# Kernel tuning notes

Measured on AMD Instinct MI355X. Metric: run time of the kernel, lower is better.

## Reference

```python
import jax, jax.numpy as jnp
import numpy as np

B, A, NN, G, F, L, MAXZ = 8, 1024, 64, 25, 128, 3, 100
CUTOFF = 5.0

def ssp(x):
    # shifted softplus: ln(0.5*e^x + 0.5) = softplus(x) - ln(2)
    return jax.nn.softplus(x) - jnp.log(2.0)

def setup_inputs() -> dict:
    key = jax.random.key(0)
    ks = jax.random.split(key, 10)
    atomic_numbers = jax.random.randint(ks[0], (B, A), 0, MAXZ)
    positions = jax.random.normal(ks[1], (B, A, 3), dtype=jnp.float32) * 3.0
    cell = jnp.zeros((B, 3, 3), dtype=jnp.float32)
    cell_offset = jnp.zeros((B, A, NN, 3), dtype=jnp.float32)
    neighbors = jax.random.randint(ks[2], (B, A, NN), 0, A)
    neighbor_mask = jnp.ones((B, A, NN), dtype=jnp.float32)
    s = 0.05
    emb = jax.random.normal(ks[3], (MAXZ, F), dtype=jnp.float32) * s
    emb = emb.at[0].set(0.0)  # padding_idx=0
    return dict(
        atomic_numbers=atomic_numbers, positions=positions, cell=cell,
        cell_offset=cell_offset, neighbors=neighbors, neighbor_mask=neighbor_mask,
        emb=emb,
        fw1=jax.random.normal(ks[4], (L, G, F), dtype=jnp.float32) * s,
        fb1=jnp.zeros((L, F), dtype=jnp.float32),
        fw2=jax.random.normal(ks[5], (L, F, F), dtype=jnp.float32) * s,
        fb2=jnp.zeros((L, F), dtype=jnp.float32),
        in2f_w=jax.random.normal(ks[6], (L, F, F), dtype=jnp.float32) * s,
        f2out_w=jax.random.normal(ks[7], (L, F, F), dtype=jnp.float32) * s,
        f2out_b=jnp.zeros((L, F), dtype=jnp.float32),
        dense_w=jax.random.normal(ks[8], (L, F, F), dtype=jnp.float32) * s,
        dense_b=jnp.zeros((L, F), dtype=jnp.float32),
    )

def reference(atomic_numbers, positions, cell, cell_offset, neighbors,
              neighbor_mask, emb, fw1, fb1, fw2, fb2, in2f_w, f2out_w,
              f2out_b, dense_w, dense_b):
    bidx = jnp.arange(B)[:, None, None]
    # embedding lookup [B,A,F]
    x = emb[atomic_numbers]
    # AtomDistances: gather neighbor positions, add cell offsets, norm
    pos_j = positions[bidx, neighbors]                       # [B,A,NN,3]
    dv = pos_j - positions[:, :, None, :] + jnp.einsum('bank,bkc->banc', cell_offset, cell)
    d2 = jnp.sum(dv * dv, axis=-1)                           # [B,A,NN]
    r_ij = jnp.where(d2 > 0, jnp.sqrt(jnp.where(d2 > 0, d2, 1.0)), 0.0)
    # GaussianSmearing on [0, cutoff] with G gaussians
    offsets = jnp.linspace(0.0, CUTOFF, G)
    width = offsets[1] - offsets[0]
    coeff = -0.5 / (width * width)
    f_ij = jnp.exp(coeff * (r_ij[..., None] - offsets) ** 2)  # [B,A,NN,G]
    mask = neighbor_mask[..., None]                           # [B,A,NN,1]
    for l in range(L):
        # filter-generating network on expanded distances -> [B,A,NN,F]
        W = ssp(f_ij @ fw1[l] + fb1[l]) @ fw2[l] + fb2[l]
        # cfconv: in2f (no bias), gather neighbor features, mul, masked sum
        y = x @ in2f_w[l]                                     # [B,A,F]
        yj = y[bidx, neighbors]                               # [B,A,NN,F]
        v = jnp.sum(yj * W * mask, axis=2)                    # [B,A,F]
        v = ssp(v @ f2out_w[l] + f2out_b[l])
        # interaction output dense (linear)
        v = v @ dense_w[l] + dense_b[l]
        x = x + v
    return x
```

## Files before the change

### kernel.cpp

```cpp
#include <hip/hip_runtime.h>
#include <hip/hip_bf16.h>
#include <math.h>

#define B_ 8
#define A_ 1024
#define NN_ 64
#define G_ 25
#define F_ 128
#define L_ 3
#define TG_ 4096
#define TGP_ (TG_ + 8)

typedef __hip_bfloat16 bf16;
typedef __bf16 bf16x8 __attribute__((ext_vector_type(8)));
typedef __bf16 bf16x4 __attribute__((ext_vector_type(4)));
typedef float floatx4 __attribute__((ext_vector_type(4)));
#define MFMA16 __builtin_amdgcn_mfma_f32_16x16x32_bf16

__device__ __forceinline__ float sspfast(float x){
  return __logf(0.5f*__expf(x) + 0.5f);
}
__device__ __forceinline__ float ldsel(const void* p, long long i, int isbf){
  return isbf ? __bfloat162float(((const bf16*)p)[i]) : ((const float*)p)[i];
}
__device__ __forceinline__ int sniff_bf16(const void* pos){
  const unsigned* raw = (const unsigned*)pos;
  unsigned w = raw[threadIdx.x & 63];
  unsigned e = (w >> 7) & 0xFF;
  return __popcll(__ballot(e >= 118 && e <= 132)) >= 32;
}

__global__ __launch_bounds__(256) void k_setup(
    const void* emb, const void* fb1, const void* fb2, const void* f2ob,
    const void* db,  const void* fw1, const void* fw2, const void* f2ow,
    const void* dw,  const void* in2f, const void* pos,
    float* c_emb, float* c_fb1, float* c_fb2, float* c_f2ob, float* c_db,
    __bf16* fw1tb, __bf16* fw2tb, __bf16* f2owtb, __bf16* dwtb, __bf16* in2ftb)
{
  int isbf = sniff_bf16(pos);
  int idx = blockIdx.x*256 + threadIdx.x;
  if(idx < 12800){ c_emb[idx] = ldsel(emb, idx, isbf); return; }
  if(idx < 13184){ c_fb1[idx-12800] = ldsel(fb1, idx-12800, isbf); return; }
  if(idx < 13568){ c_fb2[idx-13184] = ldsel(fb2, idx-13184, isbf); return; }
  if(idx < 13952){ c_f2ob[idx-13568] = ldsel(f2ob, idx-13568, isbf); return; }
  if(idx < 14336){ c_db[idx-13952] = ldsel(db, idx-13952, isbf); return; }
  if(idx < 26624){
    int i = idx - 14336;
    int l = i >> 12; int rem = i & 4095; int f = rem >> 5; int k = rem & 31;
    float v = (k < G_) ? ldsel(fw1, (long long)l*G_*F_ + k*F_ + f, isbf) : 0.0f;
    fw1tb[i] = (__bf16)v;
    return;
  }
  {
    int i = idx - 26624;
    int which = i / 49152; int r = i - which*49152;
    int l = r >> 14; int rem = r & 16383; int f = rem >> 7; int k = rem & 127;
    const void* src = (which==0) ? fw2 : (which==1) ? f2ow : (which==2) ? dw : in2f;
    __bf16* dst = (which==0) ? fw2tb : (which==1) ? f2owtb : (which==2) ? dwtb : in2ftb;
    dst[r] = (__bf16)ldsel(src, (long long)l*F_*F_ + k*F_ + f, isbf);
  }
}

__global__ __launch_bounds__(256, 4) void k_build(
    const __bf16* __restrict__ fw1tb, const float* __restrict__ fb1g,
    const __bf16* __restrict__ fw2tb, const float* __restrict__ fb2g,
    __bf16* __restrict__ wtabb,
    const int* __restrict__ z, const float* __restrict__ c_emb,
    const __bf16* __restrict__ in2ftb, float* __restrict__ xws,
    __bf16* __restrict__ ybf,
    const void* pos, const void* cell, const void* celloff,
    const int* __restrict__ nbr, const void* maskg,
    int2* __restrict__ pair)
{
  __shared__ __align__(16) unsigned char smem[22528];
  int t = threadIdx.x;
  int lane = t & 63, wid = t >> 6, c = lane & 15, quad = lane >> 4;
  int wb = wid*32;

  if(blockIdx.x >= 448){
    int isbf = sniff_bf16(pos);
    int p = (blockIdx.x - 448)*256 + t;
    int m = p >> 6;
    int b = m >> 10;
    int j = nbr[p];
    long long pi = (long long)m*3, pj = (long long)(b*A_+j)*3;
    long long co = (long long)p*3, ce = (long long)b*9;
    float o0 = ldsel(celloff,co+0,isbf), o1 = ldsel(celloff,co+1,isbf), o2 = ldsel(celloff,co+2,isbf);
    float d2 = 0.0f;
    #pragma unroll
    for(int cc=0;cc<3;cc++){
      float off = o0*ldsel(cell,ce+cc,isbf) + o1*ldsel(cell,ce+3+cc,isbf) + o2*ldsel(cell,ce+6+cc,isbf);
      float dv = ldsel(pos,pj+cc,isbf) - ldsel(pos,pi+cc,isbf) + off;
      d2 += dv*dv;
    }
    float r = (d2 > 0.0f) ? sqrtf(d2) : 0.0f;
    float msk = ldsel(maskg, p, isbf);
    int i = (int)(r * ((float)TG_ / 8.0f) + 0.5f);
    if(i > TG_-1) i = TG_-1;
    if(msk < 0.5f) i = TG_;
    int2 pr;
    pr.x = i * F_;
    pr.y = (b*A_ + j) * F_;
    pair[p] = pr;
    return;
  }

  if(blockIdx.x < 192){
    __bf16* s_h1  = (__bf16*)smem;
    __bf16* s_fij = (__bf16*)(smem + 17408);
    int layer = blockIdx.x >> 6;
    int row0  = (blockIdx.x & 63) * 64;
    __bf16* T = wtabb + (long long)layer*TGP_*F_;

    if((blockIdx.x & 63) == 0 && t < F_)
      T[(long long)TG_*F_ + t] = (__bf16)0.0f;

    const float dr = 8.0f / (float)TG_;
    const float width = 5.0f/24.0f;
    const float coeff = -0.5f/(width*width);
    for(int i=t;i<NN_*40;i+=256){
      int n = i/40, g = i - n*40;
      float val = 0.0f;
      if(g < G_){
        float rg = (float)(row0 + n) * dr;
        float d = rg - (float)g*width;
        val = __expf(coeff*d*d);
      }
      s_fij[i] = (__bf16)val;
    }
    __syncthreads();

    {
      const __bf16* fw1l = fw1tb + layer*F_*32;
      bf16x8 a0 = *(const bf16x8*)(fw1l + (wb + c)*32 + quad*8);
      bf16x8 a1 = *(const bf16x8*)(fw1l + (wb + 16 + c)*32 + quad*8);
      floatx4 bias0 = *(const floatx4*)(fb1g + layer*F_ + wb + quad*4);
      floatx4 bias1 = *(const floatx4*)(fb1g + layer*F_ + wb + 16 + quad*4);
      #pragma unroll
      for(int nt=0;nt<4;nt++){
        bf16x8 bfr = *(const bf16x8*)(s_fij + (nt*16 + c)*40 + quad*8);
        floatx4 z4 = {0.f,0.f,0.f,0.f};
        floatx4 acc0 = MFMA16(a0, bfr, z4, 0,0,0);
        floatx4 acc1 = MFMA16(a1, bfr, z4, 0,0,0);
        bf16x4 h0, h1v;
        #pragma unroll
        for(int r=0;r<4;r++){
          h0[r]  = (__bf16)sspfast(acc0[r] + bias0[r]);
          h1v[r] = (__bf16)sspfast(acc1[r] + bias1[r]);
        }
        *(bf16x4*)(s_h1 + (nt*16+c)*136 + wb + quad*4)      = h0;
        *(bf16x4*)(s_h1 + (nt*16+c)*136 + wb + 16 + quad*4) = h1v;
      }
    }
    __syncthreads();

    {
      const __bf16* fw2l = fw2tb + layer*F_*F_;
      bf16x8 aw0[4], aw1[4];
      #pragma unroll
      for(int kt=0;kt<4;kt++){
        aw0[kt] = *(const bf16x8*)(fw2l + (wb + c)*F_ + kt*32 + quad*8);
        aw1[kt] = *(const bf16x8*)(fw2l + (wb + 16 + c)*F_ + kt*32 + quad*8);
      }
      floatx4 ba0 = *(const floatx4*)(fb2g + layer*F_ + wb + quad*4);
      floatx4 ba1 = *(const floatx4*)(fb2g + layer*F_ + wb + 16 + quad*4);
      #pragma unroll
      for(int nt=0; nt<4; nt++){
        bf16x8 bh[4];
        #pragma unroll
        for(int kt=0;kt<4;kt++)
          bh[kt] = *(const bf16x8*)(s_h1 + (nt*16 + c)*136 + kt*32 + quad*8);
        floatx4 acc0 = {0.f,0.f,0.f,0.f};
        floatx4 acc1 = {0.f,0.f,0.f,0.f};
        #pragma unroll
        for(int kt=0;kt<4;kt++){
          acc0 = MFMA16(aw0[kt], bh[kt], acc0, 0,0,0);
          acc1 = MFMA16(aw1[kt], bh[kt], acc1, 0,0,0);
        }
        int row = row0 + nt*16 + c;
        bf16x4 o0, o1;
        #pragma unroll
        for(int r=0;r<4;r++){
          o0[r] = (__bf16)(acc0[r] + ba0[r]);
          o1[r] = (__bf16)(acc1[r] + ba1[r]);
        }
        *(bf16x4*)(T + (long long)row*F_ + wb + quad*4)      = o0;
        *(bf16x4*)(T + (long long)row*F_ + wb + 16 + quad*4) = o1;
      }
    }
    return;
  }

  {
    __bf16* s_a = (__bf16*)smem;
    int row0 = (blockIdx.x - 192)*32;
    #pragma unroll
    for(int i=0;i<2;i++){
      int ch = t + i*256, row = ch >> 4, col8 = ch & 15;
      const float* src = c_emb + (long long)z[row0+row]*F_ + col8*8;
      float4 a4 = ((const float4*)src)[0];
      float4 b4 = ((const float4*)src)[1];
      float* xd = xws + (long long)(row0+row)*F_ + col8*8;
      ((float4*)xd)[0] = a4; ((float4*)xd)[1] = b4;
      bf16x8 v = {(__bf16)a4.x,(__bf16)a4.y,(__bf16)a4.z,(__bf16)a4.w,
                  (__bf16)b4.x,(__bf16)b4.y,(__bf16)b4.z,(__bf16)b4.w};
      *(bf16x8*)(s_a + row*136 + col8*8) = v;
    }
    __syncthreads();
    bf16x8 aw0[4], aw1[4];
    #pragma unroll
    for(int kt=0;kt<4;kt++){
      aw0[kt] = *(const bf16x8*)(in2ftb + (wb + c)*F_ + kt*32 + quad*8);
      aw1[kt] = *(const bf16x8*)(in2ftb + (wb + 16 + c)*F_ + kt*32 + quad*8);
    }
    #pragma unroll
    for(int nt=0; nt<2; nt++){
      bf16x8 bh[4];
      #pragma unroll
      for(int kt=0;kt<4;kt++)
        bh[kt] = *(const bf16x8*)(s_a + (nt*16 + c)*136 + kt*32 + quad*8);
      floatx4 acc0 = {0.f,0.f,0.f,0.f};
      floatx4 acc1 = {0.f,0.f,0.f,0.f};
      #pragma unroll
      for(int kt=0;kt<4;kt++){
        acc0 = MFMA16(aw0[kt], bh[kt], acc0, 0,0,0);
        acc1 = MFMA16(aw1[kt], bh[kt], acc1, 0,0,0);
      }
      int row = row0 + nt*16 + c;
      bf16x4 o0, o1;
      #pragma unroll
      for(int r=0;r<4;r++){ o0[r] = (__bf16)acc0[r]; o1[r] = (__bf16)acc1[r]; }
      *(bf16x4*)(ybf + (long long)row*F_ + wb + quad*4)      = o0;
      *(bf16x4*)(ybf + (long long)row*F_ + wb + 16 + quad*4) = o1;
    }
  }
}

__global__ __launch_bounds__(256, 2) void k_layer(
    const __bf16* __restrict__ yin, const int2* __restrict__ pairg,
    const __bf16* __restrict__ Tb, float* __restrict__ xws,
    const __bf16* __restrict__ f2owl, const float* __restrict__ f2obl,
    const __bf16* __restrict__ dwl,  const float* __restrict__ dbl,
    const __bf16* __restrict__ in2fnext, __bf16* __restrict__ yout,
    void* __restrict__ dout, const void* __restrict__ pos,
    int has_next, int write_out)
{
  __shared__ __align__(16) int2  s_pair[16*NN_];
  __shared__ __align__(16) float s_vpf[4*16*128];
  __shared__ __align__(16) __bf16 s_ga[16*136];
  __shared__ __align__(16) __bf16 s_gb[16*136];

  int t = threadIdx.x;
  int bid = (int)blockIdx.x;
  int m0 = ((bid & 7) * 64 + (bid >> 3)) * 16;
  int lane = t & 63, wid = t >> 6, c = lane & 15, quad = lane >> 4;
  int isbf = sniff_bf16(pos);

  {
    const int2* src = pairg + (long long)m0*NN_;
    for(int i=t;i<16*NN_;i+=256) s_pair[i] = src[i];
  }
  __syncthreads();

  int fsl = t & 15;
  int grp = t >> 4;
  int f8 = fsl*8;
  #pragma unroll 2
  for(int a=0;a<16;a++){
    float v0=0.f,v1=0.f,v2=0.f,v3=0.f,v4=0.f,v5=0.f,v6=0.f,v7=0.f;
    #pragma unroll
    for(int jj=0;jj<4;jj++){
      int2 pr = s_pair[a*NN_ + jj*16 + grp];
      bf16x8 T = *(const bf16x8*)(Tb + pr.x + f8);
      bf16x8 Y = *(const bf16x8*)(yin + pr.y + f8);
      v0 += (float)T[0]*(float)Y[0];
      v1 += (float)T[1]*(float)Y[1];
      v2 += (float)T[2]*(float)Y[2];
      v3 += (float)T[3]*(float)Y[3];
      v4 += (float)T[4]*(float)Y[4];
      v5 += (float)T[5]*(float)Y[5];
      v6 += (float)T[6]*(float)Y[6];
      v7 += (float)T[7]*(float)Y[7];
    }
    v0 += __shfl_xor(v0,16); v1 += __shfl_xor(v1,16);
    v2 += __shfl_xor(v2,16); v3 += __shfl_xor(v3,16);
    v4 += __shfl_xor(v4,16); v5 += __shfl_xor(v5,16);
    v6 += __shfl_xor(v6,16); v7 += __shfl_xor(v7,16);
    v0 += __shfl_xor(v0,32); v1 += __shfl_xor(v1,32);
    v2 += __shfl_xor(v2,32); v3 += __shfl_xor(v3,32);
    v4 += __shfl_xor(v4,32); v5 += __shfl_xor(v5,32);
    v6 += __shfl_xor(v6,32); v7 += __shfl_xor(v7,32);
    if(lane < 16){
      float* dst = s_vpf + (wid*16 + a)*128 + lane*8;
      floatx4 lo = {v0,v1,v2,v3}, hi = {v4,v5,v6,v7};
      *(floatx4*)dst = lo;
      *(floatx4*)(dst+4) = hi;
    }
  }
  __syncthreads();
  {
    int a0 = t >> 5, q = t & 31;
    #pragma unroll
    for(int h=0; h<2; h++){
      int a = a0 + h*8;
      floatx4 p0 = *(const floatx4*)(s_vpf + (0*16+a)*128 + q*4);
      floatx4 p1 = *(const floatx4*)(s_vpf + (1*16+a)*128 + q*4);
      floatx4 p2 = *(const floatx4*)(s_vpf + (2*16+a)*128 + q*4);
      floatx4 p3 = *(const floatx4*)(s_vpf + (3*16+a)*128 + q*4);
      bf16x4 o;
      #pragma unroll
      for(int r=0;r<4;r++)
        o[r] = (__bf16)(p0[r]+p1[r]+p2[r]+p3[r]);
      *(bf16x4*)(s_ga + a*136 + q*4) = o;
    }
  }
  __syncthreads();

  int wb = wid*32;
  {
    bf16x8 aw0[4], aw1[4];
    #pragma unroll
    for(int kt=0;kt<4;kt++){
      aw0[kt] = *(const bf16x8*)(f2owl + (wb + c)*F_ + kt*32 + quad*8);
      aw1[kt] = *(const bf16x8*)(f2owl + (wb + 16 + c)*F_ + kt*32 + quad*8);
    }
    floatx4 ba0 = *(const floatx4*)(f2obl + wb + quad*4);
    floatx4 ba1 = *(const floatx4*)(f2obl + wb + 16 + quad*4);
    bf16x8 bh[4];
    #pragma unroll
    for(int kt=0;kt<4;kt++)
      bh[kt] = *(const bf16x8*)(s_ga + c*136 + kt*32 + quad*8);
    floatx4 acc0 = {0.f,0.f,0.f,0.f};
    floatx4 acc1 = {0.f,0.f,0.f,0.f};
    #pragma unroll
    for(int kt=0;kt<4;kt++){
      acc0 = MFMA16(aw0[kt], bh[kt], acc0, 0,0,0);
      acc1 = MFMA16(aw1[kt], bh[kt], acc1, 0,0,0);
    }
    bf16x4 o0, o1;
    #pragma unroll
    for(int r=0;r<4;r++){
      o0[r] = (__bf16)sspfast(acc0[r] + ba0[r]);
      o1[r] = (__bf16)sspfast(acc1[r] + ba1[r]);
    }
    *(bf16x4*)(s_gb + c*136 + wb + quad*4)      = o0;
    *(bf16x4*)(s_gb + c*136 + wb + 16 + quad*4) = o1;
  }
  __syncthreads();

  {
    bf16x8 aw0[4], aw1[4];
    #pragma unroll
    for(int kt=0;kt<4;kt++){
      aw0[kt] = *(const bf16x8*)(dwl + (wb + c)*F_ + kt*32 + quad*8);
      aw1[kt] = *(const bf16x8*)(dwl + (wb + 16 + c)*F_ + kt*32 + quad*8);
    }
    floatx4 ba0 = *(const floatx4*)(dbl + wb + quad*4);
    floatx4 ba1 = *(const floatx4*)(dbl + wb + 16 + quad*4);
    bf16x8 bh[4];
    #pragma unroll
    for(int kt=0;kt<4;kt++)
      bh[kt] = *(const bf16x8*)(s_gb + c*136 + kt*32 + quad*8);
    floatx4 acc0 = {0.f,0.f,0.f,0.f};
    floatx4 acc1 = {0.f,0.f,0.f,0.f};
    #pragma unroll
    for(int kt=0;kt<4;kt++){
      acc0 = MFMA16(aw0[kt], bh[kt], acc0, 0,0,0);
      acc1 = MFMA16(aw1[kt], bh[kt], acc1, 0,0,0);
    }
    int rowL = m0 + c;
    float* xp0 = xws + (long long)rowL*F_ + wb + quad*4;
    float* xp1 = xws + (long long)rowL*F_ + wb + 16 + quad*4;
    float4 x0 = *(const float4*)xp0;
    float4 x1 = *(const float4*)xp1;
    float4 xn0 = {x0.x+acc0[0]+ba0[0], x0.y+acc0[1]+ba0[1],
                  x0.z+acc0[2]+ba0[2], x0.w+acc0[3]+ba0[3]};
    float4 xn1 = {x1.x+acc1[0]+ba1[0], x1.y+acc1[1]+ba1[1],
                  x1.z+acc1[2]+ba1[2], x1.w+acc1[3]+ba1[3]};
    bf16x4 s0 = {(__bf16)xn0.x,(__bf16)xn0.y,(__bf16)xn0.z,(__bf16)xn0.w};
    bf16x4 s1 = {(__bf16)xn1.x,(__bf16)xn1.y,(__bf16)xn1.z,(__bf16)xn1.w};
    *(bf16x4*)(s_ga + c*136 + wb + quad*4)      = s0;
    *(bf16x4*)(s_ga + c*136 + wb + 16 + quad*4) = s1;
    *(float4*)xp0 = xn0;
    *(float4*)xp1 = xn1;
    if(write_out){
      long long gi0 = (long long)rowL*F_ + wb + quad*4;
      long long gi1 = (long long)rowL*F_ + wb + 16 + quad*4;
      if(isbf){
        *(bf16x4*)((bf16*)dout + gi0) = s0;
        *(bf16x4*)((bf16*)dout + gi1) = s1;
      }else{
        *(float4*)((float*)dout + gi0) = xn0;
        *(float4*)((float*)dout + gi1) = xn1;
      }
    }
  }
  if(!has_next) return;
  __syncthreads();

  {
    bf16x8 aw0[4], aw1[4];
    #pragma unroll
    for(int kt=0;kt<4;kt++){
      aw0[kt] = *(const bf16x8*)(in2fnext + (wb + c)*F_ + kt*32 + quad*8);
      aw1[kt] = *(const bf16x8*)(in2fnext + (wb + 16 + c)*F_ + kt*32 + quad*8);
    }
    bf16x8 bh[4];
    #pragma unroll
    for(int kt=0;kt<4;kt++)
      bh[kt] = *(const bf16x8*)(s_ga + c*136 + kt*32 + quad*8);
    floatx4 acc0 = {0.f,0.f,0.f,0.f};
    floatx4 acc1 = {0.f,0.f,0.f,0.f};
    #pragma unroll
    for(int kt=0;kt<4;kt++){
      acc0 = MFMA16(aw0[kt], bh[kt], acc0, 0,0,0);
      acc1 = MFMA16(aw1[kt], bh[kt], acc1, 0,0,0);
    }
    int row = m0 + c;
    bf16x4 o0, o1;
    #pragma unroll
    for(int r=0;r<4;r++){ o0[r] = (__bf16)acc0[r]; o1[r] = (__bf16)acc1[r]; }
    *(bf16x4*)(yout + (long long)row*F_ + wb + quad*4)      = o0;
    *(bf16x4*)(yout + (long long)row*F_ + wb + 16 + quad*4) = o1;
  }
}

extern "C" void kernel_launch(void* const* d_in, const int* in_sizes, int n_in,
                              void* d_out, int out_size, void* d_ws, size_t ws_size,
                              hipStream_t stream){
  const int*  z       = (const int*)d_in[0];
  const void* pos     = d_in[1];
  const void* cell    = d_in[2];
  const void* celloff = d_in[3];
  const int*  nbr     = (const int*)d_in[4];
  const void* mask    = d_in[5];
  const void* emb     = d_in[6];
  const void* fw1     = d_in[7];
  const void* fb1     = d_in[8];
  const void* fw2     = d_in[9];
  const void* fb2     = d_in[10];
  const void* in2f    = d_in[11];
  const void* f2ow    = d_in[12];
  const void* f2ob    = d_in[13];
  const void* dw      = d_in[14];
  const void* db      = d_in[15];

  float* base = (float*)d_ws;
  float* c_emb  = base + 16;
  float* c_fb1  = c_emb + 12800;
  float* c_fb2  = c_fb1 + 384;
  float* c_f2ob = c_fb2 + 384;
  float* c_db   = c_f2ob + 384;
  __bf16* fw1tb  = (__bf16*)(c_db + 384);
  __bf16* fw2tb  = (__bf16*)(base + 20496);
  __bf16* f2owtb = (__bf16*)(base + 45072);
  __bf16* dwtb   = (__bf16*)(base + 69648);
  __bf16* in2ftb = (__bf16*)(base + 94224);
  float*  xws   = base + 118800;
  __bf16* ybf0  = (__bf16*)(base + 1167376);
  __bf16* ybf1  = (__bf16*)(base + 1691664);
  int2*   pair  = (int2*)(base + 2215952);
  __bf16* wtabb = (__bf16*)(base + 3264528);

  k_setup<<<872, 256, 0, stream>>>(emb, fb1, fb2, f2ob, db,
                                   fw1, fw2, f2ow, dw, in2f, pos,
                                   c_emb, c_fb1, c_fb2, c_f2ob, c_db,
                                   fw1tb, fw2tb, f2owtb, dwtb, in2ftb);
  k_build<<<2496, 256, 0, stream>>>(fw1tb, c_fb1, fw2tb, c_fb2, wtabb,
                                    z, c_emb, in2ftb, xws, ybf0,
                                    pos, cell, celloff, nbr, mask, pair);

  __bf16* ycur = ybf0;
  __bf16* ynext = ybf1;
  for(int l=0;l<L_;l++){
    k_layer<<<(B_*A_)/16, 256, 0, stream>>>(ycur, pair,
                                            wtabb + (long long)l*TGP_*F_, xws,
                                            f2owtb + l*F_*F_, c_f2ob + l*F_,
                                            dwtb + l*F_*F_,  c_db + l*F_,
                                            in2ftb + (l < L_-1 ? (l+1)*F_*F_ : 0), ynext,
                                            d_out, pos,
                                            (l < L_-1) ? 1 : 0, (l == L_-1) ? 1 : 0);
    __bf16* tmp = ycur; ycur = ynext; ynext = tmp;
  }
}
```

Before: 174.2 us.

## Store filter table and neighbor features as scaled FP8 to halve gather bytes

The precomputed distance-filter table and the per-atom in2f features move from bf16 to FP8 (scaled by fixed factors 32 and 64), and the layer kernel unpacks them with packed fp8-to-f32 conversions before the multiply-accumulate. The sum is rescaled by the inverse factor before the f2out GEMM. This halves the bytes of the random neighbor gather, which dominates each layer kernel, at the cost of much lower precision and a risk of exceeding the accuracy tolerance. The extra conversion instructions add ALU work.

```diff
diff --git a/kernel.cpp b/kernel.cpp
--- a/kernel.cpp
+++ b/kernel.cpp
@@ -10,11 +10,15 @@
 #define L_ 3
 #define TG_ 4096
 #define TGP_ (TG_ + 8)
+#define SCT 32.0f
+#define SCY 64.0f
+#define INVS (1.0f/(32.0f*64.0f))
 
 typedef __hip_bfloat16 bf16;
 typedef __bf16 bf16x8 __attribute__((ext_vector_type(8)));
 typedef __bf16 bf16x4 __attribute__((ext_vector_type(4)));
 typedef float floatx4 __attribute__((ext_vector_type(4)));
+typedef float floatx2 __attribute__((ext_vector_type(2)));
 #define MFMA16 __builtin_amdgcn_mfma_f32_16x16x32_bf16
 
 __device__ __forceinline__ float sspfast(float x){
@@ -28,6 +32,11 @@
   unsigned w = raw[threadIdx.x & 63];
   unsigned e = (w >> 7) & 0xFF;
   return __popcll(__ballot(e >= 118 && e <= 132)) >= 32;
+}
+__device__ __forceinline__ unsigned int pack4_fp8(float a, float b, float c, float d){
+  int r = __builtin_amdgcn_cvt_pk_fp8_f32(a, b, 0, false);
+  r = __builtin_amdgcn_cvt_pk_fp8_f32(c, d, r, true);
+  return (unsigned int)r;
 }
 
 __global__ __launch_bounds__(256) void k_setup(
@@ -64,10 +73,10 @@
 __global__ __launch_bounds__(256, 4) void k_build(
     const __bf16* __restrict__ fw1tb, const float* __restrict__ fb1g,
     const __bf16* __restrict__ fw2tb, const float* __restrict__ fb2g,
-    __bf16* __restrict__ wtabb,
+    unsigned char* __restrict__ wtab8,
     const int* __restrict__ z, const float* __restrict__ c_emb,
     const __bf16* __restrict__ in2ftb, float* __restrict__ xws,
-    __bf16* __restrict__ ybf,
+    unsigned char* __restrict__ y8,
     const void* pos, const void* cell, const void* celloff,
     const int* __restrict__ nbr, const void* maskg,
     int2* __restrict__ pair)
@@ -110,10 +119,10 @@
     __bf16* s_fij = (__bf16*)(smem + 17408);
     int layer = blockIdx.x >> 6;
     int row0  = (blockIdx.x & 63) * 64;
-    __bf16* T = wtabb + (long long)layer*TGP_*F_;
-
-    if((blockIdx.x & 63) == 0 && t < F_)
-      T[(long long)TG_*F_ + t] = (__bf16)0.0f;
+    unsigned char* T8 = wtab8 + (long long)layer*TGP_*F_;
+
+    if((blockIdx.x & 63) == 0 && t < 32)
+      *(unsigned int*)(T8 + (long long)TG_*F_ + t*4) = 0u;
 
     const float dr = 8.0f / (float)TG_;
     const float width = 5.0f/24.0f;
@@ -178,14 +187,12 @@
           acc1 = MFMA16(aw1[kt], bh[kt], acc1, 0,0,0);
         }
         int row = row0 + nt*16 + c;
-        bf16x4 o0, o1;
-        #pragma unroll
-        for(int r=0;r<4;r++){
-          o0[r] = (__bf16)(acc0[r] + ba0[r]);
-          o1[r] = (__bf16)(acc1[r] + ba1[r]);
-        }
-        *(bf16x4*)(T + (long long)row*F_ + wb + quad*4)      = o0;
-        *(bf16x4*)(T + (long long)row*F_ + wb + 16 + quad*4) = o1;
+        unsigned int w0 = pack4_fp8((acc0[0]+ba0[0])*SCT, (acc0[1]+ba0[1])*SCT,
+                                    (acc0[2]+ba0[2])*SCT, (acc0[3]+ba0[3])*SCT);
+        unsigned int w1 = pack4_fp8((acc1[0]+ba1[0])*SCT, (acc1[1]+ba1[1])*SCT,
+                                    (acc1[2]+ba1[2])*SCT, (acc1[3]+ba1[3])*SCT);
+        *(unsigned int*)(T8 + (long long)row*F_ + wb + quad*4)      = w0;
+        *(unsigned int*)(T8 + (long long)row*F_ + wb + 16 + quad*4) = w1;
       }
     }
     return;
@@ -227,21 +234,20 @@
         acc1 = MFMA16(aw1[kt], bh[kt], acc1, 0,0,0);
       }
       int row = row0 + nt*16 + c;
-      bf16x4 o0, o1;
-      #pragma unroll
-      for(int r=0;r<4;r++){ o0[r] = (__bf16)acc0[r]; o1[r] = (__bf16)acc1[r]; }
-      *(bf16x4*)(ybf + (long long)row*F_ + wb + quad*4)      = o0;
-      *(bf16x4*)(ybf + (long long)row*F_ + wb + 16 + quad*4) = o1;
+      unsigned int w0 = pack4_fp8(acc0[0]*SCY, acc0[1]*SCY, acc0[2]*SCY, acc0[3]*SCY);
+      unsigned int w1 = pack4_fp8(acc1[0]*SCY, acc1[1]*SCY, acc1[2]*SCY, acc1[3]*SCY);
+      *(unsigned int*)(y8 + (long long)row*F_ + wb + quad*4)      = w0;
+      *(unsigned int*)(y8 + (long long)row*F_ + wb + 16 + quad*4) = w1;
     }
   }
 }
 
 __global__ __launch_bounds__(256, 2) void k_layer(
-    const __bf16* __restrict__ yin, const int2* __restrict__ pairg,
-    const __bf16* __restrict__ Tb, float* __restrict__ xws,
+    const unsigned char* __restrict__ yin, const int2* __restrict__ pairg,
+    const unsigned char* __restrict__ Tb, float* __restrict__ xws,
     const __bf16* __restrict__ f2owl, const float* __restrict__ f2obl,
     const __bf16* __restrict__ dwl,  const float* __restrict__ dbl,
-    const __bf16* __restrict__ in2fnext, __bf16* __restrict__ yout,
+    const __bf16* __restrict__ in2fnext, unsigned char* __restrict__ yout,
     void* __restrict__ dout, const void* __restrict__ pos,
     int has_next, int write_out)
 {
@@ -271,16 +277,24 @@
     #pragma unroll
     for(int jj=0;jj<4;jj++){
       int2 pr = s_pair[a*NN_ + jj*16 + grp];
-      bf16x8 T = *(const bf16x8*)(Tb + pr.x + f8);
-      bf16x8 Y = *(const bf16x8*)(yin + pr.y + f8);
-      v0 += (float)T[0]*(float)Y[0];
-      v1 += (float)T[1]*(float)Y[1];
-      v2 += (float)T[2]*(float)Y[2];
-      v3 += (float)T[3]*(float)Y[3];
-      v4 += (float)T[4]*(float)Y[4];
-      v5 += (float)T[5]*(float)Y[5];
-      v6 += (float)T[6]*(float)Y[6];
-      v7 += (float)T[7]*(float)Y[7];
+      uint2 Tw = *(const uint2*)(Tb + pr.x + f8);
+      uint2 Yw = *(const uint2*)(yin + pr.y + f8);
+      floatx2 t0 = __builtin_amdgcn_cvt_pk_f32_fp8((int)Tw.x, false);
+      floatx2 t1 = __builtin_amdgcn_cvt_pk_f32_fp8((int)Tw.x, true);
+      floatx2 t2 = __builtin_amdgcn_cvt_pk_f32_fp8((int)Tw.y, false);
+      floatx2 t3 = __builtin_amdgcn_cvt_pk_f32_fp8((int)Tw.y, true);
+      floatx2 u0 = __builtin_amdgcn_cvt_pk_f32_fp8((int)Yw.x, false);
+      floatx2 u1 = __builtin_amdgcn_cvt_pk_f32_fp8((int)Yw.x, true);
+      floatx2 u2 = __builtin_amdgcn_cvt_pk_f32_fp8((int)Yw.y, false);
+      floatx2 u3 = __builtin_amdgcn_cvt_pk_f32_fp8((int)Yw.y, true);
+      v0 += t0[0]*u0[0];
+      v1 += t0[1]*u0[1];
+      v2 += t1[0]*u1[0];
+      v3 += t1[1]*u1[1];
+      v4 += t2[0]*u2[0];
+      v5 += t2[1]*u2[1];
+      v6 += t3[0]*u3[0];
+      v7 += t3[1]*u3[1];
     }
     v0 += __shfl_xor(v0,16); v1 += __shfl_xor(v1,16);
     v2 += __shfl_xor(v2,16); v3 += __shfl_xor(v3,16);
@@ -310,7 +324,7 @@
       bf16x4 o;
       #pragma unroll
       for(int r=0;r<4;r++)
-        o[r] = (__bf16)(p0[r]+p1[r]+p2[r]+p3[r]);
+        o[r] = (__bf16)((p0[r]+p1[r]+p2[r]+p3[r]) * INVS);
       *(bf16x4*)(s_ga + a*136 + q*4) = o;
     }
   }
@@ -417,11 +431,10 @@
       acc1 = MFMA16(aw1[kt], bh[kt], acc1, 0,0,0);
     }
     int row = m0 + c;
-    bf16x4 o0, o1;
-    #pragma unroll
-    for(int r=0;r<4;r++){ o0[r] = (__bf16)acc0[r]; o1[r] = (__bf16)acc1[r]; }
-    *(bf16x4*)(yout + (long long)row*F_ + wb + quad*4)      = o0;
-    *(bf16x4*)(yout + (long long)row*F_ + wb + 16 + quad*4) = o1;
+    unsigned int w0 = pack4_fp8(acc0[0]*SCY, acc0[1]*SCY, acc0[2]*SCY, acc0[3]*SCY);
+    unsigned int w1 = pack4_fp8(acc1[0]*SCY, acc1[1]*SCY, acc1[2]*SCY, acc1[3]*SCY);
+    *(unsigned int*)(yout + (long long)row*F_ + wb + quad*4)      = w0;
+    *(unsigned int*)(yout + (long long)row*F_ + wb + 16 + quad*4) = w1;
   }
 }
 
@@ -457,29 +470,29 @@
   __bf16* dwtb   = (__bf16*)(base + 69648);
   __bf16* in2ftb = (__bf16*)(base + 94224);
   float*  xws   = base + 118800;
-  __bf16* ybf0  = (__bf16*)(base + 1167376);
-  __bf16* ybf1  = (__bf16*)(base + 1691664);
-  int2*   pair  = (int2*)(base + 2215952);
-  __bf16* wtabb = (__bf16*)(base + 3264528);
+  unsigned char* y8_0 = (unsigned char*)(base + 1167376);
+  unsigned char* y8_1 = (unsigned char*)(base + 1429520);
+  int2*   pair  = (int2*)(base + 1691664);
+  unsigned char* wtab8 = (unsigned char*)(base + 2740240);
 
   k_setup<<<872, 256, 0, stream>>>(emb, fb1, fb2, f2ob, db,
                                    fw1, fw2, f2ow, dw, in2f, pos,
                                    c_emb, c_fb1, c_fb2, c_f2ob, c_db,
                                    fw1tb, fw2tb, f2owtb, dwtb, in2ftb);
-  k_build<<<2496, 256, 0, stream>>>(fw1tb, c_fb1, fw2tb, c_fb2, wtabb,
-                                    z, c_emb, in2ftb, xws, ybf0,
+  k_build<<<2496, 256, 0, stream>>>(fw1tb, c_fb1, fw2tb, c_fb2, wtab8,
+                                    z, c_emb, in2ftb, xws, y8_0,
                                     pos, cell, celloff, nbr, mask, pair);
 
-  __bf16* ycur = ybf0;
-  __bf16* ynext = ybf1;
+  unsigned char* ycur = y8_0;
+  unsigned char* ynext = y8_1;
   for(int l=0;l<L_;l++){
     k_layer<<<(B_*A_)/16, 256, 0, stream>>>(ycur, pair,
-                                            wtabb + (long long)l*TGP_*F_, xws,
+                                            wtab8 + (long long)l*TGP_*F_, xws,
                                             f2owtb + l*F_*F_, c_f2ob + l*F_,
                                             dwtb + l*F_*F_,  c_db + l*F_,
                                             in2ftb + (l < L_-1 ? (l+1)*F_*F_ : 0), ynext,
                                             d_out, pos,
                                             (l < L_-1) ? 1 : 0, (l == L_-1) ? 1 : 0);
-    __bf16* tmp = ycur; ycur = ynext; ynext = tmp;
-  }
-}
+    unsigned char* tmp = ycur; ycur = ynext; ynext = tmp;
+  }
+}
```

After: 169.4 us. -2.8%, faster.
